# Kernel optimization log

Measured on AMD Instinct MI355X. Metric: run time of the kernel, lower is better.

The kernel has to match this reference:

```python
import jax, jax.numpy as jnp
import numpy as np

HIDDEN, BATCH, SEQ, LAYERS = 256, 32, 1024, 4


def setup_inputs() -> dict:
    key = jax.random.key(0)
    ks = jax.random.split(key, 6)
    NE = HIDDEN * BATCH
    return {
        "h_data": jax.random.normal(ks[0], ((SEQ + 1) * LAYERS * NE,), dtype=jnp.float32),
        "x_data": jax.random.normal(ks[1], (SEQ * (LAYERS + 1) * NE,), dtype=jnp.float32),
        "c_data": jax.random.normal(ks[2], ((SEQ + 1) * LAYERS * NE,), dtype=jnp.float32),
        "W": jax.random.normal(ks[3], (LAYERS, 4 * HIDDEN, HIDDEN), dtype=jnp.float32) * 0.05,
        "R": jax.random.normal(ks[4], (LAYERS, 4 * HIDDEN, HIDDEN), dtype=jnp.float32) * 0.05,
        "bias": jax.random.normal(ks[5], (LAYERS, 4 * HIDDEN), dtype=jnp.float32) * 0.05,
        "hiddenSize": HIDDEN,
        "miniBatch": BATCH,
        "seqLength": SEQ,
        "numLayers": LAYERS,
    }


def reference(h_data, x_data, c_data, W, R, bias, hiddenSize, miniBatch, seqLength, numLayers):
    NE = hiddenSize * miniBatch
    # inter-layer workspace in the CUDA code; here they are produced by scan).
    x = x_data[: seqLength * NE].reshape(seqLength, miniBatch, hiddenSize)
    h0 = h_data.reshape(numLayers, seqLength + 1, miniBatch, hiddenSize)[:, 0]
    c0 = c_data.reshape(numLayers, seqLength + 1, miniBatch, hiddenSize)[:, 0]

    inp = x
    for l in range(numLayers):
        Wl, Rl, bl = W[l], R[l], bias[l]

        def step(carry, xt, Wl=Wl, Rl=Rl, bl=bl):
            h, c = carry
            gates = xt @ Wl.T + h @ Rl.T + bl            # [B, 4H]
            i, f, g, o = jnp.split(gates, 4, axis=-1)
            i = jax.nn.sigmoid(i)
            f = jax.nn.sigmoid(f)
            g = jnp.tanh(g)
            o = jax.nn.sigmoid(o)
            c_new = f * c + i * g
            h_new = o * jnp.tanh(c_new)
            return (h_new, c_new), h_new

        _, inp = jax.lax.scan(step, (h0[l], c0[l]), inp)
    # Top-layer hidden states for all timesteps: [seqLength, miniBatch, hiddenSize]
    return inp
```

## Files before the change

kernel.cpp:

```cpp
#include <hip/hip_runtime.h>


#define HID  256
#define BAT  32
#define SEQL 1024
#define NLAY 4
#define NE   (HID*BAT)
#define WGPL 32
#define GSTR 36

typedef __attribute__((ext_vector_type(8))) short bf16x8;
typedef __attribute__((ext_vector_type(4))) float f32x4;

union U8 { bf16x8 v; unsigned short s[8]; unsigned u[4]; };

__device__ __forceinline__ unsigned short bf16_rne(float f) {
    unsigned u = __float_as_uint(f);
    u += 0x7FFFu + ((u >> 16) & 1u);
    return (unsigned short)(u >> 16);
}
__device__ __forceinline__ float bf16_to_f(unsigned short h) {
    return __uint_as_float(((unsigned)h) << 16);
}
__device__ __forceinline__ unsigned pack_hl(float f) {
    unsigned short hi = bf16_rne(f);
    unsigned short lo = bf16_rne(f - bf16_to_f(hi));
    return (((unsigned)hi) << 16) | lo;
}

__device__ __forceinline__ uint4 ld_cohx4(const unsigned* p) {
    uint4 r;
    asm volatile("global_load_dwordx4 %0, %1, off sc0 sc1" : "=v"(r) : "v"(p) : "memory");
    return r;
}
__device__ __forceinline__ void st_coh(unsigned* p, unsigned v) {
    asm volatile("global_store_dword %0, %1, off sc0 sc1" :: "v"(p), "v"(v) : "memory");
}
__device__ __forceinline__ void waitcnt0() {
    asm volatile("s_waitcnt vmcnt(0)" ::: "memory");
}

__device__ __forceinline__ float sigm(float x)  { return 1.0f / (1.0f + __expf(-x)); }
__device__ __forceinline__ float tanhx(float x) { return 1.0f - 2.0f / (__expf(2.0f * x) + 1.0f); }

__global__ __launch_bounds__(256) void pack_x(unsigned* xp) {
    int i = (blockIdx.x * 256 + threadIdx.x) * 4;
    float4 f = *(const float4*)((const float*)xp + i);
    uint4 u;
    u.x = pack_hl(f.x); u.y = pack_hl(f.y);
    u.z = pack_hl(f.z); u.w = pack_hl(f.w);
    *(uint4*)(xp + i) = u;
}

__global__ __launch_bounds__(256, 1)
void lstm_mfma(unsigned* __restrict__ hslab,
               const float* __restrict__ c_data,
               const float* __restrict__ W,
               const float* __restrict__ R,
               const float* __restrict__ bias,
               const unsigned* __restrict__ xpack,
               float* __restrict__ out,
               int* __restrict__ flags)
{
    __shared__ float ldsg[32 * GSTR];

    const int tid  = threadIdx.x;
    const int bx   = blockIdx.x;
    const int l    = bx >> 5;
    const int w    = bx & 31;

    const int wv   = tid >> 6;
    const int lane = tid & 63;
    const int mh   = wv & 1;
    const int nh   = wv >> 1;
    const int ln15 = lane & 15;
    const int kq   = lane >> 4;

    const int n_loc = nh * 16 + ln15;
    const int gate  = n_loc >> 3;
    const int uu    = n_loc & 7;
    const int grow  = gate * HID + w * 8 + uu;
    const int bg    = mh * 16 + ln15;

    const int pl = lane & 31;
    const int* fpoll = (lane < 32) ? (flags + l * 32 + pl)
                     : ((l > 0)    ? (flags + (l - 1) * 32 + pl)
                                   : (flags + pl));
    const int thr_base = (lane < 32) ? 0 : ((l > 0) ? 1 : -0x40000000);

    bf16x8 Bhi[16], Blo[16];
    {
        const float* Wl = W + (size_t)l * 4 * HID * HID;
        const float* Rl = R + (size_t)l * 4 * HID * HID;
        #pragma unroll
        for (int s = 0; s < 16; ++s) {
            int k0 = s * 32 + kq * 8;
            const float* src = (k0 < HID) ? (Wl + (size_t)grow * HID + k0)
                                          : (Rl + (size_t)grow * HID + (k0 - HID));
            float4 f0 = *(const float4*)src;
            float4 f1 = *(const float4*)(src + 4);
            float ff[8] = {f0.x, f0.y, f0.z, f0.w, f1.x, f1.y, f1.z, f1.w};
            U8 hi, lo;
            #pragma unroll
            for (int j = 0; j < 8; ++j) {
                hi.s[j] = bf16_rne(ff[j]);
                lo.s[j] = bf16_rne(ff[j] - bf16_to_f(hi.s[j]));
            }
            Bhi[s] = hi.v; Blo[s] = lo.v;
        }
    }

    const float bias_n = bias[l * 4 * HID + grow];

    const int uu2 = tid >> 5;
    const int b2  = tid & 31;
    float cst = c_data[(size_t)l * (SEQL + 1) * NE + b2 * HID + w * 8 + uu2];

    unsigned* hbuf = hslab;
    const float* h0f = (const float*)hslab + (size_t)l * (SEQL + 1) * NE;

    for (int t = 0; t < SEQL; ++t) {
        const unsigned* xsrc = (l == 0)
            ? (xpack + (size_t)t * NE)
            : (hbuf + ((size_t)(l - 1) * (SEQL + 1) + (t + 1)) * NE);

        uint4 araw[32];

        if (l == 0 && t > 0) {
            #pragma unroll
            for (int s = 0; s < 8; ++s) {
                const unsigned* p = xsrc + bg * HID + s * 32 + kq * 8;
                araw[2 * s]     = ld_cohx4(p);
                araw[2 * s + 1] = ld_cohx4(p + 4);
            }
        }

        if (wv == 0) {
            const int thr = thr_base + t;
            for (;;) {
                int v = __hip_atomic_load(fpoll, __ATOMIC_RELAXED,
                                          __HIP_MEMORY_SCOPE_AGENT);
                if (__all(v >= thr)) break;
                __builtin_amdgcn_s_sleep(1);
            }
        }
        __syncthreads();

        if (t > 0) {
            const unsigned* hsrc = hbuf + ((size_t)l * (SEQL + 1) + t) * NE;
            if (l > 0) {
                #pragma unroll
                for (int s = 0; s < 8; ++s) {
                    const unsigned* p = xsrc + bg * HID + s * 32 + kq * 8;
                    araw[2 * s]     = ld_cohx4(p);
                    araw[2 * s + 1] = ld_cohx4(p + 4);
                }
            }
            #pragma unroll
            for (int s = 8; s < 16; ++s) {
                const unsigned* p = hsrc + bg * HID + (s - 8) * 32 + kq * 8;
                araw[2 * s]     = ld_cohx4(p);
                araw[2 * s + 1] = ld_cohx4(p + 4);
            }
            asm volatile("s_waitcnt vmcnt(16)" ::: "memory");
        } else {
            #pragma unroll
            for (int s = 0; s < 8; ++s) {
                const unsigned* p = xsrc + bg * HID + s * 32 + kq * 8;
                araw[2 * s]     = ld_cohx4(p);
                araw[2 * s + 1] = ld_cohx4(p + 4);
            }
            #pragma unroll
            for (int s = 8; s < 16; ++s) {
                const float* hp = h0f + bg * HID + (s - 8) * 32 + kq * 8;
                float4 f0 = *(const float4*)hp;
                float4 f1 = *(const float4*)(hp + 4);
                uint4 a0, a1;
                a0.x = pack_hl(f0.x); a0.y = pack_hl(f0.y);
                a0.z = pack_hl(f0.z); a0.w = pack_hl(f0.w);
                a1.x = pack_hl(f1.x); a1.y = pack_hl(f1.y);
                a1.z = pack_hl(f1.z); a1.w = pack_hl(f1.w);
                araw[2 * s] = a0; araw[2 * s + 1] = a1;
            }
            waitcnt0();
        }

        f32x4 acc0 = {bias_n, bias_n, bias_n, bias_n};
        f32x4 acc1 = {0.f, 0.f, 0.f, 0.f};
        f32x4 acc2 = {0.f, 0.f, 0.f, 0.f};
        #pragma unroll
        for (int s = 0; s < 16; ++s) {
            if (s == 8 && t > 0) waitcnt0();
            uint4 d0 = araw[2 * s], d1 = araw[2 * s + 1];
            U8 ahi, alo;
            ahi.u[0] = __builtin_amdgcn_perm(d0.y, d0.x, 0x07060302u);
            ahi.u[1] = __builtin_amdgcn_perm(d0.w, d0.z, 0x07060302u);
            ahi.u[2] = __builtin_amdgcn_perm(d1.y, d1.x, 0x07060302u);
            ahi.u[3] = __builtin_amdgcn_perm(d1.w, d1.z, 0x07060302u);
            alo.u[0] = __builtin_amdgcn_perm(d0.y, d0.x, 0x05040100u);
            alo.u[1] = __builtin_amdgcn_perm(d0.w, d0.z, 0x05040100u);
            alo.u[2] = __builtin_amdgcn_perm(d1.y, d1.x, 0x05040100u);
            alo.u[3] = __builtin_amdgcn_perm(d1.w, d1.z, 0x05040100u);
            acc0 = __builtin_amdgcn_mfma_f32_16x16x32_bf16(ahi.v, Bhi[s], acc0, 0, 0, 0);
            acc1 = __builtin_amdgcn_mfma_f32_16x16x32_bf16(ahi.v, Blo[s], acc1, 0, 0, 0);
            acc2 = __builtin_amdgcn_mfma_f32_16x16x32_bf16(alo.v, Bhi[s], acc2, 0, 0, 0);
        }
        f32x4 cc = acc0 + acc1;
        cc = cc + acc2;

        *(f32x4*)&ldsg[n_loc * GSTR + mh * 16 + kq * 4] = cc;
        __syncthreads();

        float hv;
        {
            float gi = ldsg[(0 * 8 + uu2) * GSTR + b2];
            float gf = ldsg[(1 * 8 + uu2) * GSTR + b2];
            float gg = ldsg[(2 * 8 + uu2) * GSTR + b2];
            float go = ldsg[(3 * 8 + uu2) * GSTR + b2];
            float iv = sigm(gi), fv = sigm(gf), gv = tanhx(gg), ov = sigm(go);
            cst = fv * cst + iv * gv;
            hv = ov * tanhx(cst);
            unsigned dw = pack_hl(hv);
            unsigned* dst = hbuf + ((size_t)l * (SEQL + 1) + (t + 1)) * NE
                          + b2 * HID + w * 8 + uu2;
            st_coh(dst, dw);
        }
        waitcnt0();
        __syncthreads();

        if (tid == 0)
            __hip_atomic_fetch_add(&flags[l * 32 + w], 1,
                                   __ATOMIC_RELAXED, __HIP_MEMORY_SCOPE_AGENT);

        if (l == NLAY - 1)
            out[(size_t)t * NE + b2 * HID + w * 8 + uu2] = hv;
    }
}

extern "C" void kernel_launch(void* const* d_in, const int* in_sizes, int n_in,
                              void* d_out, int out_size, void* d_ws, size_t ws_size,
                              hipStream_t stream) {
    unsigned*    h_data = (unsigned*)d_in[0];
    unsigned*    x_data = (unsigned*)d_in[1];
    float*       c_data = (float*)d_in[2];
    const float* W      = (const float*)d_in[3];
    const float* R      = (const float*)d_in[4];
    const float* bias   = (const float*)d_in[5];
    float* out = (float*)d_out;

    const size_t flag_bytes = (size_t)NLAY * WGPL * sizeof(int);
    int* flags;
    if (ws_size >= flag_bytes) flags = (int*)d_ws;
    else                       flags = (int*)(c_data + NE);
    hipMemsetAsync(flags, 0, flag_bytes, stream);

    pack_x<<<dim3(8192), dim3(256), 0, stream>>>(x_data);

    lstm_mfma<<<dim3(NLAY * WGPL), dim3(256), 0, stream>>>(
        h_data, c_data, W, R, bias, x_data, out, flags);
}
```

Before: 6.805 ms.

## Replace flag counters with data-embedded valid bits for inter-block LSTM sync

Drops the per-workgroup flag counters and the atomic increment/poll handshake. Each stored hidden value now carries a valid bit in its low mantissa bit, and consumers spin on the data loads themselves until every word has the bit set. The host memsets the hidden-state slabs to zero before each run so the bit is clear initially. This removes a flag round trip, a store-drain wait and a barrier per timestep. In exchange every launch now pays for a large memset, and forcing the low bit perturbs the lo-part of the packed bf16 pair slightly.

Result: slower. 9.197 ms (+35.2%).

```diff
diff --git a/kernel.cpp b/kernel.cpp
--- a/kernel.cpp
+++ b/kernel.cpp
@@ -11,6 +11,7 @@
 
 typedef __attribute__((ext_vector_type(8))) short bf16x8;
 typedef __attribute__((ext_vector_type(4))) float f32x4;
+typedef unsigned long long u64;
 
 union U8 { bf16x8 v; unsigned short s[8]; unsigned u[4]; };
 
@@ -28,20 +29,29 @@
     return (((unsigned)hi) << 16) | lo;
 }
 
-__device__ __forceinline__ uint4 ld_cohx4(const unsigned* p) {
-    uint4 r;
-    asm volatile("global_load_dwordx4 %0, %1, off sc0 sc1" : "=v"(r) : "v"(p) : "memory");
-    return r;
-}
-__device__ __forceinline__ void st_coh(unsigned* p, unsigned v) {
-    asm volatile("global_store_dword %0, %1, off sc0 sc1" :: "v"(p), "v"(v) : "memory");
-}
-__device__ __forceinline__ void waitcnt0() {
-    asm volatile("s_waitcnt vmcnt(0)" ::: "memory");
-}
-
 __device__ __forceinline__ float sigm(float x)  { return 1.0f / (1.0f + __expf(-x)); }
 __device__ __forceinline__ float tanhx(float x) { return 1.0f - 2.0f / (__expf(2.0f * x) + 1.0f); }
+
+__device__ __forceinline__ void mfma_step(u64 q0, u64 q1, u64 q2, u64 q3,
+                                          bf16x8 bh, bf16x8 bl,
+                                          f32x4& a0, f32x4& a1, f32x4& a2) {
+    unsigned d0 = (unsigned)q0, d1 = (unsigned)(q0 >> 32);
+    unsigned d2 = (unsigned)q1, d3 = (unsigned)(q1 >> 32);
+    unsigned d4 = (unsigned)q2, d5 = (unsigned)(q2 >> 32);
+    unsigned d6 = (unsigned)q3, d7 = (unsigned)(q3 >> 32);
+    U8 ahi, alo;
+    ahi.u[0] = __builtin_amdgcn_perm(d1, d0, 0x07060302u);
+    ahi.u[1] = __builtin_amdgcn_perm(d3, d2, 0x07060302u);
+    ahi.u[2] = __builtin_amdgcn_perm(d5, d4, 0x07060302u);
+    ahi.u[3] = __builtin_amdgcn_perm(d7, d6, 0x07060302u);
+    alo.u[0] = __builtin_amdgcn_perm(d1, d0, 0x05040100u);
+    alo.u[1] = __builtin_amdgcn_perm(d3, d2, 0x05040100u);
+    alo.u[2] = __builtin_amdgcn_perm(d5, d4, 0x05040100u);
+    alo.u[3] = __builtin_amdgcn_perm(d7, d6, 0x05040100u);
+    a0 = __builtin_amdgcn_mfma_f32_16x16x32_bf16(ahi.v, bh, a0, 0, 0, 0);
+    a1 = __builtin_amdgcn_mfma_f32_16x16x32_bf16(ahi.v, bl, a1, 0, 0, 0);
+    a2 = __builtin_amdgcn_mfma_f32_16x16x32_bf16(alo.v, bh, a2, 0, 0, 0);
+}
 
 __global__ __launch_bounds__(256) void pack_x(unsigned* xp) {
     int i = (blockIdx.x * 256 + threadIdx.x) * 4;
@@ -59,8 +69,7 @@
                const float* __restrict__ R,
                const float* __restrict__ bias,
                const unsigned* __restrict__ xpack,
-               float* __restrict__ out,
-               int* __restrict__ flags)
+               float* __restrict__ out)
 {
     __shared__ float ldsg[32 * GSTR];
 
@@ -81,12 +90,6 @@
     const int uu    = n_loc & 7;
     const int grow  = gate * HID + w * 8 + uu;
     const int bg    = mh * 16 + ln15;
-
-    const int pl = lane & 31;
-    const int* fpoll = (lane < 32) ? (flags + l * 32 + pl)
-                     : ((l > 0)    ? (flags + (l - 1) * 32 + pl)
-                                   : (flags + pl));
-    const int thr_base = (lane < 32) ? 0 : ((l > 0) ? 1 : -0x40000000);
 
     bf16x8 Bhi[16], Blo[16];
     {
@@ -123,93 +126,89 @@
         const unsigned* xsrc = (l == 0)
             ? (xpack + (size_t)t * NE)
             : (hbuf + ((size_t)(l - 1) * (SEQL + 1) + (t + 1)) * NE);
-
-        uint4 araw[32];
-
-        if (l == 0 && t > 0) {
-            #pragma unroll
-            for (int s = 0; s < 8; ++s) {
-                const unsigned* p = xsrc + bg * HID + s * 32 + kq * 8;
-                araw[2 * s]     = ld_cohx4(p);
-                araw[2 * s + 1] = ld_cohx4(p + 4);
-            }
-        }
-
-        if (wv == 0) {
-            const int thr = thr_base + t;
-            for (;;) {
-                int v = __hip_atomic_load(fpoll, __ATOMIC_RELAXED,
-                                          __HIP_MEMORY_SCOPE_AGENT);
-                if (__all(v >= thr)) break;
-                __builtin_amdgcn_s_sleep(1);
-            }
-        }
-        __syncthreads();
-
-        if (t > 0) {
-            const unsigned* hsrc = hbuf + ((size_t)l * (SEQL + 1) + t) * NE;
-            if (l > 0) {
-                #pragma unroll
-                for (int s = 0; s < 8; ++s) {
-                    const unsigned* p = xsrc + bg * HID + s * 32 + kq * 8;
-                    araw[2 * s]     = ld_cohx4(p);
-                    araw[2 * s + 1] = ld_cohx4(p + 4);
-                }
-            }
-            #pragma unroll
-            for (int s = 8; s < 16; ++s) {
-                const unsigned* p = hsrc + bg * HID + (s - 8) * 32 + kq * 8;
-                araw[2 * s]     = ld_cohx4(p);
-                araw[2 * s + 1] = ld_cohx4(p + 4);
-            }
-            asm volatile("s_waitcnt vmcnt(16)" ::: "memory");
-        } else {
-            #pragma unroll
-            for (int s = 0; s < 8; ++s) {
-                const unsigned* p = xsrc + bg * HID + s * 32 + kq * 8;
-                araw[2 * s]     = ld_cohx4(p);
-                araw[2 * s + 1] = ld_cohx4(p + 4);
-            }
-            #pragma unroll
-            for (int s = 8; s < 16; ++s) {
-                const float* hp = h0f + bg * HID + (s - 8) * 32 + kq * 8;
-                float4 f0 = *(const float4*)hp;
-                float4 f1 = *(const float4*)(hp + 4);
-                uint4 a0, a1;
-                a0.x = pack_hl(f0.x); a0.y = pack_hl(f0.y);
-                a0.z = pack_hl(f0.z); a0.w = pack_hl(f0.w);
-                a1.x = pack_hl(f1.x); a1.y = pack_hl(f1.y);
-                a1.z = pack_hl(f1.z); a1.w = pack_hl(f1.w);
-                araw[2 * s] = a0; araw[2 * s + 1] = a1;
-            }
-            waitcnt0();
-        }
+        const unsigned* hsrc = hbuf + ((size_t)l * (SEQL + 1) + t) * NE;
 
         f32x4 acc0 = {bias_n, bias_n, bias_n, bias_n};
         f32x4 acc1 = {0.f, 0.f, 0.f, 0.f};
         f32x4 acc2 = {0.f, 0.f, 0.f, 0.f};
-        #pragma unroll
-        for (int s = 0; s < 16; ++s) {
-            if (s == 8 && t > 0) waitcnt0();
-            uint4 d0 = araw[2 * s], d1 = araw[2 * s + 1];
-            U8 ahi, alo;
-            ahi.u[0] = __builtin_amdgcn_perm(d0.y, d0.x, 0x07060302u);
-            ahi.u[1] = __builtin_amdgcn_perm(d0.w, d0.z, 0x07060302u);
-            ahi.u[2] = __builtin_amdgcn_perm(d1.y, d1.x, 0x07060302u);
-            ahi.u[3] = __builtin_amdgcn_perm(d1.w, d1.z, 0x07060302u);
-            alo.u[0] = __builtin_amdgcn_perm(d0.y, d0.x, 0x05040100u);
-            alo.u[1] = __builtin_amdgcn_perm(d0.w, d0.z, 0x05040100u);
-            alo.u[2] = __builtin_amdgcn_perm(d1.y, d1.x, 0x05040100u);
-            alo.u[3] = __builtin_amdgcn_perm(d1.w, d1.z, 0x05040100u);
-            acc0 = __builtin_amdgcn_mfma_f32_16x16x32_bf16(ahi.v, Bhi[s], acc0, 0, 0, 0);
-            acc1 = __builtin_amdgcn_mfma_f32_16x16x32_bf16(ahi.v, Blo[s], acc1, 0, 0, 0);
-            acc2 = __builtin_amdgcn_mfma_f32_16x16x32_bf16(alo.v, Bhi[s], acc2, 0, 0, 0);
-        }
+
+        {
+            u64 xq[32];
+            if (l == 0) {
+                #pragma unroll
+                for (int s = 0; s < 8; ++s) {
+                    const u64* p = (const u64*)(xsrc + bg * HID + s * 32 + kq * 8);
+                    #pragma unroll
+                    for (int j = 0; j < 4; ++j) xq[4 * s + j] = p[j];
+                }
+            } else {
+                int tries = 0;
+                for (;;) {
+                    unsigned m = 0xFFFFFFFFu;
+                    #pragma unroll
+                    for (int s = 0; s < 8; ++s) {
+                        const u64* p = (const u64*)(xsrc + bg * HID + s * 32 + kq * 8);
+                        #pragma unroll
+                        for (int j = 0; j < 4; ++j) {
+                            u64 v = __hip_atomic_load(p + j, __ATOMIC_RELAXED,
+                                                      __HIP_MEMORY_SCOPE_AGENT);
+                            xq[4 * s + j] = v;
+                            m &= (unsigned)v & (unsigned)(v >> 32);
+                        }
+                    }
+                    if (__all((m & 1u) != 0u)) break;
+                    if (++tries > 4) __builtin_amdgcn_s_sleep(1);
+                }
+            }
+            #pragma unroll
+            for (int s = 0; s < 8; ++s)
+                mfma_step(xq[4 * s], xq[4 * s + 1], xq[4 * s + 2], xq[4 * s + 3],
+                          Bhi[s], Blo[s], acc0, acc1, acc2);
+        }
+
+        {
+            u64 hq[32];
+            if (t == 0) {
+                #pragma unroll
+                for (int s = 0; s < 8; ++s) {
+                    const float* hp = h0f + bg * HID + s * 32 + kq * 8;
+                    #pragma unroll
+                    for (int j = 0; j < 4; ++j) {
+                        float2 f = *(const float2*)(hp + 2 * j);
+                        hq[4 * s + j] = (u64)pack_hl(f.x)
+                                      | ((u64)pack_hl(f.y) << 32);
+                    }
+                }
+            } else {
+                int tries = 0;
+                for (;;) {
+                    unsigned m = 0xFFFFFFFFu;
+                    #pragma unroll
+                    for (int s = 0; s < 8; ++s) {
+                        const u64* p = (const u64*)(hsrc + bg * HID + s * 32 + kq * 8);
+                        #pragma unroll
+                        for (int j = 0; j < 4; ++j) {
+                            u64 v = __hip_atomic_load(p + j, __ATOMIC_RELAXED,
+                                                      __HIP_MEMORY_SCOPE_AGENT);
+                            hq[4 * s + j] = v;
+                            m &= (unsigned)v & (unsigned)(v >> 32);
+                        }
+                    }
+                    if (__all((m & 1u) != 0u)) break;
+                    if (++tries > 16) __builtin_amdgcn_s_sleep(1);
+                }
+            }
+            #pragma unroll
+            for (int s = 0; s < 8; ++s)
+                mfma_step(hq[4 * s], hq[4 * s + 1], hq[4 * s + 2], hq[4 * s + 3],
+                          Bhi[8 + s], Blo[8 + s], acc0, acc1, acc2);
+        }
+
         f32x4 cc = acc0 + acc1;
         cc = cc + acc2;
 
         *(f32x4*)&ldsg[n_loc * GSTR + mh * 16 + kq * 4] = cc;
-        __syncthreads();
+        asm volatile("s_waitcnt lgkmcnt(0)\n\ts_barrier" ::: "memory");
 
         float hv;
         {
@@ -220,20 +219,16 @@
             float iv = sigm(gi), fv = sigm(gf), gv = tanhx(gg), ov = sigm(go);
             cst = fv * cst + iv * gv;
             hv = ov * tanhx(cst);
-            unsigned dw = pack_hl(hv);
+            unsigned dw = pack_hl(hv) | 1u;
             unsigned* dst = hbuf + ((size_t)l * (SEQL + 1) + (t + 1)) * NE
                           + b2 * HID + w * 8 + uu2;
-            st_coh(dst, dw);
-        }
-        waitcnt0();
-        __syncthreads();
-
-        if (tid == 0)
-            __hip_atomic_fetch_add(&flags[l * 32 + w], 1,
-                                   __ATOMIC_RELAXED, __HIP_MEMORY_SCOPE_AGENT);
-
+            __hip_atomic_store(dst, dw, __ATOMIC_RELAXED,
+                               __HIP_MEMORY_SCOPE_AGENT);
+        }
         if (l == NLAY - 1)
             out[(size_t)t * NE + b2 * HID + w * 8 + uu2] = hv;
+
+        asm volatile("s_barrier" ::: "memory");
     }
 }
 
@@ -248,14 +243,13 @@
     const float* bias   = (const float*)d_in[5];
     float* out = (float*)d_out;
 
-    const size_t flag_bytes = (size_t)NLAY * WGPL * sizeof(int);
-    int* flags;
-    if (ws_size >= flag_bytes) flags = (int*)d_ws;
-    else                       flags = (int*)(c_data + NE);
-    hipMemsetAsync(flags, 0, flag_bytes, stream);
+    for (int l = 0; l < NLAY; ++l) {
+        unsigned* slot1 = h_data + ((size_t)l * (SEQL + 1) + 1) * NE;
+        hipMemsetAsync(slot1, 0, (size_t)SEQL * NE * sizeof(unsigned), stream);
+    }
 
     pack_x<<<dim3(8192), dim3(256), 0, stream>>>(x_data);
 
     lstm_mfma<<<dim3(NLAY * WGPL), dim3(256), 0, stream>>>(
-        h_data, c_data, W, R, bias, x_data, out, flags);
-}
+        h_data, c_data, W, R, bias, x_data, out);
+}
```
